# Optimization experiments

Hardware: AMD Instinct MI355X
Metric: run time of the kernel (lower is better)

The kernel has to match this reference:

```python
import jax, jax.numpy as jnp
import numpy as np

B, T, D = 2, 2048, 1024
H = 16
HD = D // H
NE = 17  # n_edge_types + 1

def setup_inputs() -> dict:
    key = jax.random.key(0)
    ks = jax.random.split(key, 6)
    x = jax.random.normal(ks[0], (B, T, D), dtype=jnp.float32)
    graph_adj = jax.random.uniform(ks[1], (B, T, T), dtype=jnp.float32)
    edge_types = jax.random.randint(ks[2], (B, T, T), 0, NE, dtype=jnp.int32)
    Wqkv = jax.random.normal(ks[3], (D, 3 * D), dtype=jnp.float32) * (D ** -0.5)
    Wproj = jax.random.normal(ks[4], (D, D), dtype=jnp.float32) * (D ** -0.5)
    adj_bias = jnp.zeros((H,), dtype=jnp.float32)
    edge_table = jax.random.normal(ks[5], (NE, H), dtype=jnp.float32) * 0.02
    return {"x": x, "graph_adj": graph_adj, "edge_types": edge_types,
            "Wqkv": Wqkv, "Wproj": Wproj, "adj_bias": adj_bias,
            "edge_table": edge_table}

def reference(x, graph_adj, edge_types, Wqkv, Wproj, adj_bias, edge_table):
    Bc, Tc, C = x.shape
    qkv = (x @ Wqkv).reshape(Bc, Tc, 3, H, HD)
    q, k, v = qkv[:, :, 0], qkv[:, :, 1], qkv[:, :, 2]  # [B,T,H,HD]
    scale = 1.0 / jnp.sqrt(jnp.asarray(HD, dtype=x.dtype))
    # scores: [B,H,T,T]
    attn = jnp.einsum('bqhd,bkhd->bhqk', q, k) * scale
    # adjacency bias per head
    attn = attn + adj_bias[None, :, None, None] * graph_adj[:, None, :, :]
    # edge-type bias: lookup [B,T,T,H] -> [B,H,T,T]
    etype_b = edge_table[edge_types]  # [B,T,T,H]
    attn = attn + jnp.transpose(etype_b, (0, 3, 1, 2))
    # causal mask (upper triangle, diag=1)
    causal = jnp.triu(jnp.ones((Tc, Tc), dtype=bool), k=1)
    attn = jnp.where(causal[None, None, :, :], jnp.asarray(-jnp.inf, dtype=attn.dtype), attn)
    attn = jax.nn.softmax(attn, axis=-1)
    out = jnp.einsum('bhqk,bkhd->bqhd', attn, v).reshape(Bc, Tc, C)
    return out @ Wproj
```

## Files before the change

kernel.cpp:

```cpp
#include <hip/hip_runtime.h>
#include <stdint.h>

#define TT 2048
#define HH 16
#define LOG2E 1.44269504089f

typedef _Float16 f16;
typedef __attribute__((ext_vector_type(8))) _Float16 f16x8;
typedef __attribute__((ext_vector_type(4))) float f32x4;
typedef unsigned short ushort_t;

__device__ __forceinline__ void gl_lds16(const void* g, void* l){
  __builtin_amdgcn_global_load_lds(
      (__attribute__((address_space(1))) void*)(void*)g,
      (__attribute__((address_space(3))) void*)l, 16, 0, 0);
}

__device__ __forceinline__ void lds_barrier(){
  __asm__ volatile("s_waitcnt lgkmcnt(0)\n\ts_barrier" ::: "memory");
}

struct SchedT { unsigned short v[80]; };
static constexpr SchedT make_sched(){
  SchedT s{};
  int idx = 0;
  for (int size = 8; size >= 1; --size){
    for (int qt = 31; qt >= 8; --qt){
      int full = qt >> 3;
      int tail = (qt & 7) + 1;
      if (size == 8)
        for (int ci = 0; ci < full; ++ci)
          s.v[idx++] = (unsigned short)(qt | (ci << 8));
      if (tail == size)
        s.v[idx++] = (unsigned short)(qt | (full << 8));
    }
    s.v[idx++] = (unsigned short)(size - 1);
  }
  return s;
}
__constant__ SchedT SCHED = make_sched();

__device__ __forceinline__ int slot_base(int qt){
  return (qt < 16) ? 2 * (qt - 8)
       : (qt < 24) ? 16 + 3 * (qt - 16)
                   : 40 + 4 * (qt - 24);
}

__global__ __launch_bounds__(256) void cvt_f2h_kernel(const float4* __restrict__ in,
                                                      uint2* __restrict__ out, int n4){
  int i = blockIdx.x * 256 + threadIdx.x;
  if (i >= n4) return;
  float4 v = in[i];
  union { f16 h[4]; uint2 u; } o;
  o.h[0] = (f16)v.x; o.h[1] = (f16)v.y; o.h[2] = (f16)v.z; o.h[3] = (f16)v.w;
  out[i] = o.u;
}

__global__ __launch_bounds__(256) void pack_bias_kernel(const float* __restrict__ gadj,
                                                        const int* __restrict__ etype,
                                                        uint32_t* __restrict__ out){
  int bid = blockIdx.x;
  int b = bid / 528, ti = bid - b * 528;
  int qt = (int)((sqrtf(8.f * (float)ti + 1.f) - 1.f) * 0.5f);
  while ((qt + 1) * (qt + 2) / 2 <= ti) ++qt;
  while (qt * (qt + 1) / 2 > ti) --qt;
  int kt = ti - qt * (qt + 1) / 2;

  int t = threadIdx.x;
  int row = t >> 2, c0 = (t & 3) << 4;
  size_t src = ((size_t)b * TT + qt * 64 + row) * TT + kt * 64 + c0;
  uint32_t* dst = out + (size_t)bid * 4096;
  int wq = (row >> 4) * 64 + ((row & 15) >> 2) * 16;
  int jbase = (t & 3) * 4 + (row & 3);
  #pragma unroll
  for (int v4 = 0; v4 < 4; ++v4){
    float4 g = *(const float4*)(gadj + src + v4 * 4);
    int4   e = *(const int4*)(etype + src + v4 * 4);
    union { f16 h; ushort_t u; } c;
    c.h = (f16)g.x; dst[(wq + v4 * 4 + 0) * 16 + jbase] = (uint32_t)c.u | ((uint32_t)e.x << 16);
    c.h = (f16)g.y; dst[(wq + v4 * 4 + 1) * 16 + jbase] = (uint32_t)c.u | ((uint32_t)e.y << 16);
    c.h = (f16)g.z; dst[(wq + v4 * 4 + 2) * 16 + jbase] = (uint32_t)c.u | ((uint32_t)e.z << 16);
    c.h = (f16)g.w; dst[(wq + v4 * 4 + 3) * 16 + jbase] = (uint32_t)c.u | ((uint32_t)e.w << 16);
  }
}

__global__ __launch_bounds__(256) void transpose_cvt_kernel(const float* __restrict__ in,
                                                            f16* __restrict__ out, int R, int C){
  __shared__ float tile[64][65];
  int c0 = blockIdx.x * 64, r0 = blockIdx.y * 64;
  int t = threadIdx.x;
  int row = t >> 2, cs = (t & 3) << 4;
  const float4* src = (const float4*)(in + (size_t)(r0 + row) * C + c0 + cs);
  float4 a = src[0], b = src[1], c = src[2], d = src[3];
  float* tr = &tile[row][cs];
  tr[0]=a.x; tr[1]=a.y; tr[2]=a.z;  tr[3]=a.w;
  tr[4]=b.x; tr[5]=b.y; tr[6]=b.z;  tr[7]=b.w;
  tr[8]=c.x; tr[9]=c.y; tr[10]=c.z; tr[11]=c.w;
  tr[12]=d.x;tr[13]=d.y;tr[14]=d.z; tr[15]=d.w;
  __syncthreads();
  f16 tmp[16];
  #pragma unroll
  for (int j = 0; j < 16; ++j) tmp[j] = (f16)tile[cs + j][row];
  f16* dst = out + (size_t)(c0 + row) * R + r0 + cs;
  *(uint4*)dst = *(uint4*)&tmp[0];
  *(uint4*)(dst + 8) = *(uint4*)&tmp[8];
}

__global__ __launch_bounds__(256) void gemm_f16_kernel(const f16* __restrict__ A,
                                                       const f16* __restrict__ Bt,
                                                       void* __restrict__ Cout,
                                                       int M, int N, int K, int out_f32){
  __shared__ __align__(16) f16 As[128 * 32];
  __shared__ __align__(16) f16 Bs[128 * 32];
  int t = threadIdx.x;
  int w = t >> 6, lane = t & 63;
  int wm = (w >> 1) * 64, wn = (w & 1) * 64;
  int lrow = lane & 15, quad = lane >> 4;
  int bm = blockIdx.y, bn = blockIdx.x;

  f32x4 acc[4][4];
  for (int i = 0; i < 4; ++i)
    for (int j = 0; j < 4; ++j)
      for (int r = 0; r < 4; ++r) acc[i][j][r] = 0.f;

  const int nk = K >> 5;
  for (int kt = 0; kt < nk; ++kt){
    int k0 = kt << 5;
    __syncthreads();
    #pragma unroll
    for (int i = 0; i < 2; ++i){
      int c = (w << 7) + (i << 6) + lane;
      gl_lds16(A  + (size_t)((bm << 7) + (c >> 2)) * K + k0 + ((c & 3) << 3),
               As + ((w << 7) + (i << 6)) * 8);
      gl_lds16(Bt + (size_t)((bn << 7) + (c >> 2)) * K + k0 + ((c & 3) << 3),
               Bs + ((w << 7) + (i << 6)) * 8);
    }
    __syncthreads();
    f16x8 af[4], bfr[4];
    #pragma unroll
    for (int mi = 0; mi < 4; ++mi)
      af[mi] = *(const f16x8*)(As + (wm + mi * 16 + lrow) * 32 + quad * 8);
    #pragma unroll
    for (int ni = 0; ni < 4; ++ni)
      bfr[ni] = *(const f16x8*)(Bs + (wn + ni * 16 + lrow) * 32 + quad * 8);
    #pragma unroll
    for (int mi = 0; mi < 4; ++mi)
      #pragma unroll
      for (int ni = 0; ni < 4; ++ni)
        acc[mi][ni] = __builtin_amdgcn_mfma_f32_16x16x32_f16(af[mi], bfr[ni], acc[mi][ni], 0, 0, 0);
  }

  #pragma unroll
  for (int mi = 0; mi < 4; ++mi)
    #pragma unroll
    for (int ni = 0; ni < 4; ++ni)
      #pragma unroll
      for (int r = 0; r < 4; ++r){
        int row = (bm << 7) + wm + mi * 16 + quad * 4 + r;
        int col = (bn << 7) + wn + ni * 16 + lrow;
        float val = acc[mi][ni][r];
        if (out_f32) ((float*)Cout)[(size_t)row * N + col] = val;
        else         ((f16*)Cout)[(size_t)row * N + col] = (f16)val;
      }
}

__global__ __launch_bounds__(256, 4) void attn_kernel(const f16* __restrict__ qkv,
                                                      const uint32_t* __restrict__ pbias,
                                                      const float* __restrict__ adj_bias,
                                                      const float* __restrict__ edge_table,
                                                      f16* __restrict__ attn_out,
                                                      f16* __restrict__ Opart,
                                                      float* __restrict__ MLpart){
  __shared__ __align__(16) f16 Ks[64 * 72];
  __shared__ __align__(16) f16 Vt[64 * 72];
  __shared__ __align__(16) f16 Ps[4][16 * 72];
  __shared__ float edge_lds[8 * 33];

  int bx = blockIdx.x;
  int bh = bx & 31;
  int h = bh & 15, b = bh >> 4;
  int ej = SCHED.v[bx >> 5];
  int qt = ej & 31, ci = ej >> 8;
  int ksrt = ci << 3;
  int kend = min(qt, ksrt + 7);
  bool whole = (qt < 8);

  int t = threadIdx.x;
  int w = t >> 6, lane = t & 63;
  int lrow = lane & 15, quad = lane >> 4;

  if (t < 136){
    int cp = t / 17, e = t - cp * 17;
    edge_lds[cp * 33 + e] = edge_table[e * HH + h] * LOG2E;
  }
  float adjb = adj_bias[h] * LOG2E;
  int erep = (lane & 7) * 33;

  int q0 = qt * 64 + w * 16;
  const size_t qrow = ((size_t)b * TT + q0 + lrow) * 3072 + h * 64;
  f16x8 qf0 = *(const f16x8*)(qkv + qrow + quad * 8);
  f16x8 qf1 = *(const f16x8*)(qkv + qrow + 32 + quad * 8);

  f32x4 o[4];
  for (int i = 0; i < 4; ++i)
    for (int r = 0; r < 4; ++r) o[i][r] = 0.f;
  float mrun[4] = {-1e30f, -1e30f, -1e30f, -1e30f};
  float lrun[4] = {0.f, 0.f, 0.f, 0.f};

  const int keyA = t >> 3,        hdA = (t & 7) << 3;
  const int keyB = 32 + (t >> 3), hdB = hdA;
  const int sA = ((keyA >> 3) ^ (hdA >> 3)) & 7;
  const int sB = ((keyB >> 3) ^ (hdB >> 3)) & 7;
  const f16* kbase = qkv + (size_t)b * TT * 3072 + 1024 + h * 64;
  const f16* vbase = qkv + (size_t)b * TT * 3072 + 2048 + h * 64;
  const size_t koffA = (size_t)keyA * 3072 + hdA;
  const size_t koffB = (size_t)keyB * 3072 + hdB;

  const float SCL = 0.125f * LOG2E;

  const int tribase = b * 528 + ((qt * (qt + 1)) >> 1);
  const uint32_t* bthread = pbias + ((size_t)t << 4);
  const int qgb = q0 + quad * 4;

  uint4 ka, kb, va, vb;
  {
    const f16* kr = kbase + (size_t)(ksrt * 64) * 3072;
    const f16* vr = vbase + (size_t)(ksrt * 64) * 3072;
    ka = *(const uint4*)(kr + koffA); kb = *(const uint4*)(kr + koffB);
    va = *(const uint4*)(vr + koffA); vb = *(const uint4*)(vr + koffB);
  }

  for (int kt2 = ksrt; kt2 <= kend; ++kt2){
    lds_barrier();
    union B4 { uint4 v; uint32_t e[4]; } bb0, bb1, bb2, bb3;
    {
      const uint32_t* tp = bthread + ((size_t)(tribase + kt2) << 12);
      bb0.v = *(const uint4*)(tp + 0);
      bb1.v = *(const uint4*)(tp + 4);
      bb2.v = *(const uint4*)(tp + 8);
      bb3.v = *(const uint4*)(tp + 12);
    }
    *(uint4*)(Ks + keyA * 72 + hdA) = ka;
    *(uint4*)(Ks + keyB * 72 + hdB) = kb;
    {
      union { uint4 u; f16 hh[8]; } ua, ub;
      ua.u = va; ub.u = vb;
      #pragma unroll
      for (int jj = 0; jj < 8; ++jj){
        Vt[(hdA + jj) * 72 + (sA << 3) + (keyA & 7)] = ua.hh[jj];
        Vt[(hdB + jj) * 72 + (sB << 3) + (keyB & 7)] = ub.hh[jj];
      }
    }
    if (kt2 < kend){
      const f16* kr = kbase + (size_t)((kt2 + 1) * 64) * 3072;
      const f16* vr = vbase + (size_t)((kt2 + 1) * 64) * 3072;
      ka = *(const uint4*)(kr + koffA); kb = *(const uint4*)(kr + koffB);
      va = *(const uint4*)(vr + koffA); vb = *(const uint4*)(vr + koffB);
    }
    lds_barrier();

    f32x4 sf[4];
    #pragma unroll
    for (int nb = 0; nb < 4; ++nb){
      f32x4 s = {0.f, 0.f, 0.f, 0.f};
      f16x8 kf0 = *(const f16x8*)(Ks + (nb * 16 + lrow) * 72 + quad * 8);
      f16x8 kf1 = *(const f16x8*)(Ks + (nb * 16 + lrow) * 72 + 32 + quad * 8);
      s = __builtin_amdgcn_mfma_f32_16x16x32_f16(qf0, kf0, s, 0, 0, 0);
      s = __builtin_amdgcn_mfma_f32_16x16x32_f16(qf1, kf1, s, 0, 0, 0);
      sf[nb] = s;
    }

    int kgb = kt2 * 64 + lrow;
    float sarr[4][4];
    bool diag = (kt2 == qt);
#define MASK_NB(nb, BB)                                                          \
    {                                                                            \
      int kg = kgb + nb * 16;                                                    \
      _Pragma("unroll")                                                          \
      for (int r = 0; r < 4; ++r){                                               \
        float v;                                                                 \
        if (diag && kg > qgb + r) v = -1e30f;                                    \
        else {                                                                   \
          uint32_t bp = BB.e[r];                                                 \
          union { ushort_t u; f16 h; } cv; cv.u = (ushort_t)bp;                  \
          v = sf[nb][r] * SCL + adjb * (float)cv.h + edge_lds[erep + (bp >> 16)];\
        }                                                                        \
        sarr[nb][r] = v;                                                         \
      }                                                                          \
    }
    MASK_NB(0, bb0)
    MASK_NB(1, bb1)
    MASK_NB(2, bb2)
    MASK_NB(3, bb3)
#undef MASK_NB

    float mx[4];
    bool need = false;
    #pragma unroll
    for (int r = 0; r < 4; ++r){
      float m_ = fmaxf(fmaxf(sarr[0][r], sarr[1][r]), fmaxf(sarr[2][r], sarr[3][r]));
      m_ = fmaxf(m_, __shfl_xor(m_, 1));
      m_ = fmaxf(m_, __shfl_xor(m_, 2));
      m_ = fmaxf(m_, __shfl_xor(m_, 4));
      m_ = fmaxf(m_, __shfl_xor(m_, 8));
      mx[r] = m_;
      need = need || (m_ > mrun[r] + 5.0f);
    }
    if (__any(need)){
      #pragma unroll
      for (int r = 0; r < 4; ++r){
        float mnew = fmaxf(mrun[r], mx[r]);
        float alpha = exp2f(mrun[r] - mnew);
        lrun[r] *= alpha;
        #pragma unroll
        for (int nbh = 0; nbh < 4; ++nbh) o[nbh][r] *= alpha;
        mrun[r] = mnew;
      }
    }
    float pv_[4][4];
    #pragma unroll
    for (int r = 0; r < 4; ++r){
      float rs = 0.f;
      #pragma unroll
      for (int nb = 0; nb < 4; ++nb){
        float p = exp2f(sarr[nb][r] - mrun[r]);
        pv_[nb][r] = p; rs += p;
      }
      rs += __shfl_xor(rs, 1); rs += __shfl_xor(rs, 2);
      rs += __shfl_xor(rs, 4); rs += __shfl_xor(rs, 8);
      lrun[r] += rs;
    }

    f16* Pw = &Ps[w][0];
    #pragma unroll
    for (int nb = 0; nb < 4; ++nb)
      #pragma unroll
      for (int r = 0; r < 4; ++r)
        Pw[(quad * 4 + r) * 72 + nb * 16 + lrow] = (f16)pv_[nb][r];
    __asm__ volatile("s_waitcnt lgkmcnt(0)" ::: "memory");

    #pragma unroll
    for (int cc = 0; cc < 2; ++cc){
      f16x8 pf = *(const f16x8*)(Pw + lrow * 72 + cc * 32 + quad * 8);
      #pragma unroll
      for (int nbh = 0; nbh < 4; ++nbh){
        int hd = nbh * 16 + lrow;
        int sb = (hd >> 3) & 7;
        f16x8 vf = *(const f16x8*)(Vt + hd * 72 + (((cc * 4 + quad) ^ sb) << 3));
        o[nbh] = __builtin_amdgcn_mfma_f32_16x16x32_f16(pf, vf, o[nbh], 0, 0, 0);
      }
    }
  }

  if (whole){
    float inv[4];
    #pragma unroll
    for (int r = 0; r < 4; ++r) inv[r] = 1.0f / lrun[r];
    #pragma unroll
    for (int nbh = 0; nbh < 4; ++nbh)
      #pragma unroll
      for (int r = 0; r < 4; ++r){
        int qg = q0 + quad * 4 + r;
        int col = h * 64 + nbh * 16 + lrow;
        attn_out[((size_t)b * TT + qg) * 1024 + col] = (f16)(o[nbh][r] * inv[r]);
      }
  } else {
    int slot = bh * 72 + slot_base(qt) + ci;
    f16* Ob = Opart + (size_t)slot * 4096;
    #pragma unroll
    for (int nbh = 0; nbh < 4; ++nbh)
      #pragma unroll
      for (int r = 0; r < 4; ++r)
        Ob[(w * 16 + quad * 4 + r) * 64 + nbh * 16 + lrow] = (f16)o[nbh][r];
    if (lrow == 0){
      #pragma unroll
      for (int r = 0; r < 4; ++r){
        int qq = w * 16 + quad * 4 + r;
        MLpart[(size_t)slot * 128 + qq] = mrun[r];
        MLpart[(size_t)slot * 128 + 64 + qq] = lrun[r];
      }
    }
  }
}

__global__ __launch_bounds__(256) void combine_kernel(const f16* __restrict__ Opart,
                                                      const float* __restrict__ ML,
                                                      f16* __restrict__ attn_out){
  int qt = blockIdx.x + 8;
  int bh = blockIdx.y;
  int nch = (qt >> 3) + 1;
  int slot0 = bh * 72 + slot_base(qt);
  int t = threadIdx.x;
  int q = t >> 2;
  int hd0 = (t & 3) << 4;

  float m[4], l[4];
  float M = -1e30f;
  #pragma unroll
  for (int c = 0; c < 4; ++c){
    if (c < nch){
      m[c] = ML[(size_t)(slot0 + c) * 128 + q];
      l[c] = ML[(size_t)(slot0 + c) * 128 + 64 + q];
      M = fmaxf(M, m[c]);
    } else { m[c] = -1e30f; l[c] = 0.f; }
  }
  float acc[16];
  #pragma unroll
  for (int i = 0; i < 16; ++i) acc[i] = 0.f;
  float L = 0.f;
  #pragma unroll
  for (int c = 0; c < 4; ++c){
    if (c < nch){
      float wgt = exp2f(m[c] - M);
      L += l[c] * wgt;
      const f16* O = Opart + (size_t)(slot0 + c) * 4096 + q * 64 + hd0;
      f16x8 a0 = *(const f16x8*)O, a1 = *(const f16x8*)(O + 8);
      #pragma unroll
      for (int i = 0; i < 8; ++i){
        acc[i]     += (float)a0[i] * wgt;
        acc[i + 8] += (float)a1[i] * wgt;
      }
    }
  }
  float invL = 1.0f / L;
  f16 outv[16];
  #pragma unroll
  for (int i = 0; i < 16; ++i) outv[i] = (f16)(acc[i] * invL);
  int b = bh >> 4, h = bh & 15;
  f16* dst = attn_out + ((size_t)b * TT + qt * 64 + q) * 1024 + h * 64 + hd0;
  *(uint4*)dst = *(uint4*)&outv[0];
  *(uint4*)(dst + 8) = *(uint4*)&outv[8];
}

extern "C" void kernel_launch(void* const* d_in, const int* in_sizes, int n_in,
                              void* d_out, int out_size, void* d_ws, size_t ws_size,
                              hipStream_t stream){
  (void)in_sizes; (void)n_in; (void)out_size; (void)ws_size;
  const float* x_f32  = (const float*)d_in[0];
  const float* gadj   = (const float*)d_in[1];
  const int*   etype  = (const int*)d_in[2];
  const float* wqkv   = (const float*)d_in[3];
  const float* wproj  = (const float*)d_in[4];
  const float* adjb   = (const float*)d_in[5];
  const float* etab   = (const float*)d_in[6];

  char* ws = (char*)d_ws;
  f16*     x_f16  = (f16*)(ws);
  f16*     qkv    = (f16*)(ws + (8u  << 20));
  f16*     wqkvT  = (f16*)(ws + (32u << 20));
  f16*     Opart  = (f16*)(ws + (32u << 20));
  f16*     wprojT = (f16*)(ws + (51u << 20));
  float*   MLpart = (float*)(ws + (53u << 20));
  uint32_t* pbias = (uint32_t*)(ws + (55u << 20));
  f16*     attn_o = x_f16;

  cvt_f2h_kernel<<<4096, 256, 0, stream>>>((const float4*)x_f32, (uint2*)x_f16, 1048576);
  pack_bias_kernel<<<1056, 256, 0, stream>>>(gadj, etype, pbias);
  transpose_cvt_kernel<<<dim3(48, 16), 256, 0, stream>>>(wqkv, wqkvT, 1024, 3072);
  transpose_cvt_kernel<<<dim3(16, 16), 256, 0, stream>>>(wproj, wprojT, 1024, 1024);
  gemm_f16_kernel<<<dim3(24, 32), 256, 0, stream>>>(x_f16, wqkvT, qkv, 4096, 3072, 1024, 0);
  attn_kernel<<<2560, 256, 0, stream>>>(qkv, pbias, adjb, etab, attn_o, Opart, MLpart);
  combine_kernel<<<dim3(24, 32), 256, 0, stream>>>(Opart, MLpart, attn_o);
  gemm_f16_kernel<<<dim3(8, 32), 256, 0, stream>>>(attn_o, wprojT, d_out, 4096, 1024, 1024, 1);
}
```

Measured before the change: 295.7 us.

## Use DPP row reductions, wider edge-table replication, and paired-key V transpose stores

Replaces the shfl_xor-based max and sum row reductions in the attention softmax with DPP quad_perm and row_ror moves, avoiding LDS-routed permutes. Replicates the per-head edge-bias table 32 ways instead of 8 to cut LDS bank conflicts on the per-element lookup. Each thread now stages two adjacent keys instead of keys 32 apart, so the V transpose into LDS packs two f16 values into one 32-bit store, halving the number of scattered stores. It costs a little more LDS for the edge table and changes the global-load pattern for K/V staging.

```diff
diff --git a/kernel.cpp b/kernel.cpp
--- a/kernel.cpp
+++ b/kernel.cpp
@@ -18,6 +18,27 @@
 
 __device__ __forceinline__ void lds_barrier(){
   __asm__ volatile("s_waitcnt lgkmcnt(0)\n\ts_barrier" ::: "memory");
+}
+
+template<int CTRL>
+__device__ __forceinline__ float dpp_mov(float x){
+  int xi = __builtin_bit_cast(int, x);
+  return __builtin_bit_cast(float,
+      __builtin_amdgcn_update_dpp(xi, xi, CTRL, 0xF, 0xF, false));
+}
+__device__ __forceinline__ float row_red_max(float x){
+  x = fmaxf(x, dpp_mov<0xB1>(x));
+  x = fmaxf(x, dpp_mov<0x4E>(x));
+  x = fmaxf(x, dpp_mov<0x124>(x));
+  x = fmaxf(x, dpp_mov<0x128>(x));
+  return x;
+}
+__device__ __forceinline__ float row_red_sum(float x){
+  x += dpp_mov<0xB1>(x);
+  x += dpp_mov<0x4E>(x);
+  x += dpp_mov<0x124>(x);
+  x += dpp_mov<0x128>(x);
+  return x;
 }
 
 struct SchedT { unsigned short v[80]; };
@@ -174,7 +195,7 @@
   __shared__ __align__(16) f16 Ks[64 * 72];
   __shared__ __align__(16) f16 Vt[64 * 72];
   __shared__ __align__(16) f16 Ps[4][16 * 72];
-  __shared__ float edge_lds[8 * 33];
+  __shared__ float edge_lds[32 * 17];
 
   int bx = blockIdx.x;
   int bh = bx & 31;
@@ -189,12 +210,10 @@
   int w = t >> 6, lane = t & 63;
   int lrow = lane & 15, quad = lane >> 4;
 
-  if (t < 136){
-    int cp = t / 17, e = t - cp * 17;
-    edge_lds[cp * 33 + e] = edge_table[e * HH + h] * LOG2E;
-  }
+  for (int i = t; i < 544; i += 256)
+    edge_lds[i] = edge_table[(i % 17) * HH + h] * LOG2E;
   float adjb = adj_bias[h] * LOG2E;
-  int erep = (lane & 7) * 33;
+  int erep = (lane & 31) * 17;
 
   int q0 = qt * 64 + w * 16;
   const size_t qrow = ((size_t)b * TT + q0 + lrow) * 3072 + h * 64;
@@ -207,14 +226,13 @@
   float mrun[4] = {-1e30f, -1e30f, -1e30f, -1e30f};
   float lrun[4] = {0.f, 0.f, 0.f, 0.f};
 
-  const int keyA = t >> 3,        hdA = (t & 7) << 3;
-  const int keyB = 32 + (t >> 3), hdB = hdA;
-  const int sA = ((keyA >> 3) ^ (hdA >> 3)) & 7;
-  const int sB = ((keyB >> 3) ^ (hdB >> 3)) & 7;
+  const int keyA = (t >> 3) << 1;
+  const int hdA  = (t & 7) << 3;
+  const int sA   = ((keyA >> 3) ^ (hdA >> 3)) & 7;
   const f16* kbase = qkv + (size_t)b * TT * 3072 + 1024 + h * 64;
   const f16* vbase = qkv + (size_t)b * TT * 3072 + 2048 + h * 64;
   const size_t koffA = (size_t)keyA * 3072 + hdA;
-  const size_t koffB = (size_t)keyB * 3072 + hdB;
+  const size_t koffB = koffA + 3072;
 
   const float SCL = 0.125f * LOG2E;
 
@@ -241,14 +259,15 @@
       bb3.v = *(const uint4*)(tp + 12);
     }
     *(uint4*)(Ks + keyA * 72 + hdA) = ka;
-    *(uint4*)(Ks + keyB * 72 + hdB) = kb;
+    *(uint4*)(Ks + (keyA + 1) * 72 + hdA) = kb;
     {
       union { uint4 u; f16 hh[8]; } ua, ub;
       ua.u = va; ub.u = vb;
       #pragma unroll
       for (int jj = 0; jj < 8; ++jj){
-        Vt[(hdA + jj) * 72 + (sA << 3) + (keyA & 7)] = ua.hh[jj];
-        Vt[(hdB + jj) * 72 + (sB << 3) + (keyB & 7)] = ub.hh[jj];
+        union { f16 h[2]; uint32_t wv; } pr;
+        pr.h[0] = ua.hh[jj]; pr.h[1] = ub.hh[jj];
+        *(uint32_t*)(Vt + (hdA + jj) * 72 + (sA << 3) + (keyA & 7)) = pr.wv;
       }
     }
     if (kt2 < kend){
@@ -299,10 +318,7 @@
     #pragma unroll
     for (int r = 0; r < 4; ++r){
       float m_ = fmaxf(fmaxf(sarr[0][r], sarr[1][r]), fmaxf(sarr[2][r], sarr[3][r]));
-      m_ = fmaxf(m_, __shfl_xor(m_, 1));
-      m_ = fmaxf(m_, __shfl_xor(m_, 2));
-      m_ = fmaxf(m_, __shfl_xor(m_, 4));
-      m_ = fmaxf(m_, __shfl_xor(m_, 8));
+      m_ = row_red_max(m_);
       mx[r] = m_;
       need = need || (m_ > mrun[r] + 5.0f);
     }
@@ -326,8 +342,7 @@
         float p = exp2f(sarr[nb][r] - mrun[r]);
         pv_[nb][r] = p; rs += p;
       }
-      rs += __shfl_xor(rs, 1); rs += __shfl_xor(rs, 2);
-      rs += __shfl_xor(rs, 4); rs += __shfl_xor(rs, 8);
+      rs = row_red_sum(rs);
       lrun[r] += rs;
     }
 
```

Result: faster. 282.9 us (-4.3%).
